# Performance work log

Hardware: AMD Instinct MI355X
Metric: run time of the kernel (lower is better)

The kernel has to match this reference:

```python
import jax, jax.numpy as jnp
import numpy as np

N = 1_000_000
D1 = 16          # n_input_1 (first-layer features, cols 0:16)
D2 = 16          # n_input_2 (second-layer features, cols 16:32)
NC = 64          # n_clusters (first layer)
NCPC = 8         # n_clusters_per_cluster (second layer)


def setup_inputs() -> dict:
    key = jax.random.key(0)
    k1, k2, k3 = jax.random.split(key, 3)
    x = jax.random.normal(k1, (N, D1 + D2), dtype=jnp.float32)
    centers_outer = jax.random.normal(k2, (NC, D1), dtype=jnp.float32)
    centers_inner = jax.random.normal(k3, (NC, NCPC, D2), dtype=jnp.float32)
    return {"x": x, "centers_outer": centers_outer, "centers_inner": centers_inner}


def reference(x, centers_outer, centers_inner):
    # x: [N, D1+D2]; input_1_idx = cols [0:D1], input_2_idx = cols [D1:D1+D2]
    x1 = x[:, :D1]
    x2 = x[:, D1:]

    # First-layer nearest-centroid assignment (squared Euclidean).
    # ||x1 - c||^2 = ||x1||^2 - 2 x1.c + ||c||^2; the ||x1||^2 term is
    # constant over clusters so it does not affect the argmin.
    d1 = jnp.sum(centers_outer ** 2, axis=-1)[None, :] - 2.0 * (x1 @ centers_outer.T)  # [N, NC]
    outer = jnp.argmin(d1, axis=1)  # [N] int

    # Second-layer assignment: each sample only compares against the NCPC
    # sub-centers of its outer cluster (this fuses the original per-cluster
    # torch.where gather/scatter loop into one vectorized pass).
    sub = centers_inner[outer]  # [N, NCPC, D2] gather
    d2 = jnp.sum(sub ** 2, axis=-1) - 2.0 * jnp.einsum("nd,nkd->nk", x2, sub)  # [N, NCPC]
    inner = jnp.argmin(d2, axis=1)  # [N]

    return inner + outer * NCPC  # combined cluster id in [0, NC*NCPC)
```

## Files before the change

### kernel.cpp

```cpp
#include <hip/hip_runtime.h>

constexpr int D = 16;
constexpr int NC = 64;
constexpr int NCPC = 8;
constexpr int OSTRIDE = NCPC * D + 4;
constexpr int NPT = 4;
constexpr int BLOCK = 256;

__global__ __launch_bounds__(BLOCK, 4)
void cluster_kernel(const float* __restrict__ x,
                    const float* __restrict__ co,
                    const float* __restrict__ ci,
                    int* __restrict__ out, int n)
{
    __shared__ __align__(16) float s_ci[NC * OSTRIDE];
    __shared__ __align__(16) float s_onorm[NC];
    __shared__ float s_inorm[NC * 9];

    const int t = threadIdx.x;

    const float4* ci4 = (const float4*)ci;
#pragma unroll
    for (int i = 0; i < 8; ++i) {
        int idx = t + i * BLOCK;
        int o = idx >> 5;
        int f = idx & 31;
        *(float4*)&s_ci[o * OSTRIDE + f * 4] = ci4[idx];
    }
    for (int i = t; i < NC + NC * NCPC; i += BLOCK) {
        const float* src = (i < NC) ? (co + i * D) : (ci + (size_t)(i - NC) * D);
        float s = 0.f;
#pragma unroll
        for (int k = 0; k < D; ++k) s = fmaf(src[k], src[k], s);
        if (i < NC) s_onorm[i] = s;
        else { int ii = i - NC; s_inorm[(ii >> 3) * 9 + (ii & 7)] = s; }
    }
    __syncthreads();

    const int base = blockIdx.x * (BLOCK * NPT) + t;

    int p[NPT];
    bool valid[NPT];
#pragma unroll
    for (int pt = 0; pt < NPT; ++pt) {
        int pp = base + pt * BLOCK;
        valid[pt] = pp < n;
        p[pt] = valid[pt] ? pp : (n - 1);
    }

    float x1[NPT][D];
#pragma unroll
    for (int pt = 0; pt < NPT; ++pt) {
        const float4* xp = (const float4*)(x + (size_t)p[pt] * 32);
        float4 a = xp[0], b = xp[1], c = xp[2], d = xp[3];
        x1[pt][0]=a.x;  x1[pt][1]=a.y;  x1[pt][2]=a.z;  x1[pt][3]=a.w;
        x1[pt][4]=b.x;  x1[pt][5]=b.y;  x1[pt][6]=b.z;  x1[pt][7]=b.w;
        x1[pt][8]=c.x;  x1[pt][9]=c.y;  x1[pt][10]=c.z; x1[pt][11]=c.w;
        x1[pt][12]=d.x; x1[pt][13]=d.y; x1[pt][14]=d.z; x1[pt][15]=d.w;
    }

    float bestd[NPT]; int bo[NPT];
#pragma unroll
    for (int pt = 0; pt < NPT; ++pt) { bestd[pt] = 3.4e38f; bo[pt] = 0; }

#pragma unroll 2
    for (int j = 0; j < NC; ++j) {
        float cj[D];
#pragma unroll
        for (int k = 0; k < D; ++k) cj[k] = co[j * D + k];
        float nrm = s_onorm[j];
#pragma unroll
        for (int pt = 0; pt < NPT; ++pt) {
            float dot = 0.f;
#pragma unroll
            for (int k = 0; k < D; ++k) dot = fmaf(x1[pt][k], cj[k], dot);
            float dd = fmaf(-2.f, dot, nrm);
            if (dd < bestd[pt]) { bestd[pt] = dd; bo[pt] = j; }
        }
    }

#pragma unroll
    for (int pt = 0; pt < NPT; ++pt) {
        const float4* xp = (const float4*)(x + (size_t)p[pt] * 32);
        float4 a = xp[4], b = xp[5], c = xp[6], d = xp[7];
        float x2[D] = {a.x,a.y,a.z,a.w, b.x,b.y,b.z,b.w,
                       c.x,c.y,c.z,c.w, d.x,d.y,d.z,d.w};
        const float* cb = s_ci + bo[pt] * OSTRIDE;
        const float* nb = s_inorm + bo[pt] * 9;
        float bd = 3.4e38f; int bk = 0;
#pragma unroll
        for (int k = 0; k < NCPC; ++k) {
            float4 c0 = *(const float4*)&cb[k * D + 0];
            float4 c1 = *(const float4*)&cb[k * D + 4];
            float4 c2 = *(const float4*)&cb[k * D + 8];
            float4 c3 = *(const float4*)&cb[k * D + 12];
            float dot = 0.f;
            dot = fmaf(x2[0],  c0.x, dot); dot = fmaf(x2[1],  c0.y, dot);
            dot = fmaf(x2[2],  c0.z, dot); dot = fmaf(x2[3],  c0.w, dot);
            dot = fmaf(x2[4],  c1.x, dot); dot = fmaf(x2[5],  c1.y, dot);
            dot = fmaf(x2[6],  c1.z, dot); dot = fmaf(x2[7],  c1.w, dot);
            dot = fmaf(x2[8],  c2.x, dot); dot = fmaf(x2[9],  c2.y, dot);
            dot = fmaf(x2[10], c2.z, dot); dot = fmaf(x2[11], c2.w, dot);
            dot = fmaf(x2[12], c3.x, dot); dot = fmaf(x2[13], c3.y, dot);
            dot = fmaf(x2[14], c3.z, dot); dot = fmaf(x2[15], c3.w, dot);
            float dd = fmaf(-2.f, dot, nb[k]);
            if (dd < bd) { bd = dd; bk = k; }
        }
        if (valid[pt]) out[p[pt]] = bo[pt] * NCPC + bk;
    }
}

extern "C" void kernel_launch(void* const* d_in, const int* in_sizes, int n_in,
                              void* d_out, int out_size, void* d_ws, size_t ws_size,
                              hipStream_t stream) {
    const float* x  = (const float*)d_in[0];
    const float* co = (const float*)d_in[1];
    const float* ci = (const float*)d_in[2];
    int* out = (int*)d_out;
    int n = in_sizes[0] / 32;
    int blocks = (n + BLOCK * NPT - 1) / (BLOCK * NPT);
    cluster_kernel<<<blocks, BLOCK, 0, stream>>>(x, co, ci, out, n);
}
```

Measured before the change: 205.0 us.

## Prefetch outer centroids, broadcast norms via readlane, load full rows upfront

```diff
diff --git a/kernel.cpp b/kernel.cpp
--- a/kernel.cpp
+++ b/kernel.cpp
@@ -4,8 +4,12 @@
 constexpr int NC = 64;
 constexpr int NCPC = 8;
 constexpr int OSTRIDE = NCPC * D + 4;
-constexpr int NPT = 4;
+constexpr int NPT = 2;
 constexpr int BLOCK = 256;
+
+__device__ __forceinline__ float lane_bcast(float v, int lane) {
+    return __int_as_float(__builtin_amdgcn_readlane(__float_as_int(v), lane));
+}
 
 __global__ __launch_bounds__(BLOCK, 4)
 void cluster_kernel(const float* __restrict__ x,
@@ -14,7 +18,7 @@
                     int* __restrict__ out, int n)
 {
     __shared__ __align__(16) float s_ci[NC * OSTRIDE];
-    __shared__ __align__(16) float s_onorm[NC];
+    __shared__ float s_onorm[NC];
     __shared__ float s_inorm[NC * 9];
 
     const int t = threadIdx.x;
@@ -37,10 +41,10 @@
     }
     __syncthreads();
 
+    float mynorm = s_onorm[t & 63];
+
     const int base = blockIdx.x * (BLOCK * NPT) + t;
-
-    int p[NPT];
-    bool valid[NPT];
+    int p[NPT]; bool valid[NPT];
 #pragma unroll
     for (int pt = 0; pt < NPT; ++pt) {
         int pp = base + pt * BLOCK;
@@ -48,43 +52,51 @@
         p[pt] = valid[pt] ? pp : (n - 1);
     }
 
-    float x1[NPT][D];
+    float x1[NPT][D], x2[NPT][D];
 #pragma unroll
     for (int pt = 0; pt < NPT; ++pt) {
         const float4* xp = (const float4*)(x + (size_t)p[pt] * 32);
         float4 a = xp[0], b = xp[1], c = xp[2], d = xp[3];
+        float4 e = xp[4], f = xp[5], g = xp[6], h = xp[7];
         x1[pt][0]=a.x;  x1[pt][1]=a.y;  x1[pt][2]=a.z;  x1[pt][3]=a.w;
         x1[pt][4]=b.x;  x1[pt][5]=b.y;  x1[pt][6]=b.z;  x1[pt][7]=b.w;
         x1[pt][8]=c.x;  x1[pt][9]=c.y;  x1[pt][10]=c.z; x1[pt][11]=c.w;
         x1[pt][12]=d.x; x1[pt][13]=d.y; x1[pt][14]=d.z; x1[pt][15]=d.w;
+        x2[pt][0]=e.x;  x2[pt][1]=e.y;  x2[pt][2]=e.z;  x2[pt][3]=e.w;
+        x2[pt][4]=f.x;  x2[pt][5]=f.y;  x2[pt][6]=f.z;  x2[pt][7]=f.w;
+        x2[pt][8]=g.x;  x2[pt][9]=g.y;  x2[pt][10]=g.z; x2[pt][11]=g.w;
+        x2[pt][12]=h.x; x2[pt][13]=h.y; x2[pt][14]=h.z; x2[pt][15]=h.w;
     }
 
     float bestd[NPT]; int bo[NPT];
 #pragma unroll
     for (int pt = 0; pt < NPT; ++pt) { bestd[pt] = 3.4e38f; bo[pt] = 0; }
 
+    float cur[D];
+#pragma unroll
+    for (int k = 0; k < D; ++k) cur[k] = co[k];
+
 #pragma unroll 2
     for (int j = 0; j < NC; ++j) {
-        float cj[D];
+        float nxt[D];
+        int jn = (j < NC - 1) ? (j + 1) : j;
 #pragma unroll
-        for (int k = 0; k < D; ++k) cj[k] = co[j * D + k];
-        float nrm = s_onorm[j];
+        for (int k = 0; k < D; ++k) nxt[k] = co[jn * D + k];
+        float nrm = lane_bcast(mynorm, j);
 #pragma unroll
         for (int pt = 0; pt < NPT; ++pt) {
             float dot = 0.f;
 #pragma unroll
-            for (int k = 0; k < D; ++k) dot = fmaf(x1[pt][k], cj[k], dot);
+            for (int k = 0; k < D; ++k) dot = fmaf(x1[pt][k], cur[k], dot);
             float dd = fmaf(-2.f, dot, nrm);
             if (dd < bestd[pt]) { bestd[pt] = dd; bo[pt] = j; }
         }
+#pragma unroll
+        for (int k = 0; k < D; ++k) cur[k] = nxt[k];
     }
 
 #pragma unroll
     for (int pt = 0; pt < NPT; ++pt) {
-        const float4* xp = (const float4*)(x + (size_t)p[pt] * 32);
-        float4 a = xp[4], b = xp[5], c = xp[6], d = xp[7];
-        float x2[D] = {a.x,a.y,a.z,a.w, b.x,b.y,b.z,b.w,
-                       c.x,c.y,c.z,c.w, d.x,d.y,d.z,d.w};
         const float* cb = s_ci + bo[pt] * OSTRIDE;
         const float* nb = s_inorm + bo[pt] * 9;
         float bd = 3.4e38f; int bk = 0;
@@ -95,14 +107,14 @@
             float4 c2 = *(const float4*)&cb[k * D + 8];
             float4 c3 = *(const float4*)&cb[k * D + 12];
             float dot = 0.f;
-            dot = fmaf(x2[0],  c0.x, dot); dot = fmaf(x2[1],  c0.y, dot);
-            dot = fmaf(x2[2],  c0.z, dot); dot = fmaf(x2[3],  c0.w, dot);
-            dot = fmaf(x2[4],  c1.x, dot); dot = fmaf(x2[5],  c1.y, dot);
-            dot = fmaf(x2[6],  c1.z, dot); dot = fmaf(x2[7],  c1.w, dot);
-            dot = fmaf(x2[8],  c2.x, dot); dot = fmaf(x2[9],  c2.y, dot);
-            dot = fmaf(x2[10], c2.z, dot); dot = fmaf(x2[11], c2.w, dot);
-            dot = fmaf(x2[12], c3.x, dot); dot = fmaf(x2[13], c3.y, dot);
-            dot = fmaf(x2[14], c3.z, dot); dot = fmaf(x2[15], c3.w, dot);
+            dot = fmaf(x2[pt][0],  c0.x, dot); dot = fmaf(x2[pt][1],  c0.y, dot);
+            dot = fmaf(x2[pt][2],  c0.z, dot); dot = fmaf(x2[pt][3],  c0.w, dot);
+            dot = fmaf(x2[pt][4],  c1.x, dot); dot = fmaf(x2[pt][5],  c1.y, dot);
+            dot = fmaf(x2[pt][6],  c1.z, dot); dot = fmaf(x2[pt][7],  c1.w, dot);
+            dot = fmaf(x2[pt][8],  c2.x, dot); dot = fmaf(x2[pt][9],  c2.y, dot);
+            dot = fmaf(x2[pt][10], c2.z, dot); dot = fmaf(x2[pt][11], c2.w, dot);
+            dot = fmaf(x2[pt][12], c3.x, dot); dot = fmaf(x2[pt][13], c3.y, dot);
+            dot = fmaf(x2[pt][14], c3.z, dot); dot = fmaf(x2[pt][15], c3.w, dot);
             float dd = fmaf(-2.f, dot, nb[k]);
             if (dd < bd) { bd = dd; bk = k; }
         }
```

After: 200.1 us. 1.02x faster.
